# Kernel optimization log

Hardware: AMD Instinct MI355X
Metric: run time of the kernel (lower is better)

The kernel has to match this reference:

```python
import jax, jax.numpy as jnp
import numpy as np

B, S, D_IN = 1, 1024, 2048
H_QK, H_V, DK, DV = 8, 16, 128, 128
KCONV = 4
D_OUT = H_QK * DK          # 1024
D_OUT_VG = H_V * DV        # 2048
FUSED = 2 * D_OUT + D_OUT_VG  # 4096
EPS = 1e-6


def setup_inputs() -> dict:
    key = jax.random.key(0)
    ks = jax.random.split(key, 8)
    return {
        "x": jax.random.normal(ks[0], (B, S, D_IN), jnp.float32),
        "w_qkv": jax.random.normal(ks[1], (FUSED, D_IN), jnp.float32) * 0.02,
        "w_gate": jax.random.normal(ks[2], (D_OUT_VG, D_IN), jnp.float32) * 0.02,
        "w_beta": jax.random.normal(ks[3], (H_V, D_IN), jnp.float32) * 0.02,
        "w_alpha": jax.random.normal(ks[4], (H_V, D_IN), jnp.float32) * 0.02,
        "log_A": jnp.log(jax.random.uniform(ks[5], (H_V,), jnp.float32, 1e-3, 16.0)),
        "dt_bias": jnp.ones((H_V,), jnp.float32),
        "conv_w": jax.random.normal(ks[6], (FUSED, 1, KCONV), jnp.float32) * 0.1,
        "rms_w": jnp.ones((DV,), jnp.float32),
        "w_out": jax.random.normal(ks[7], (D_IN, D_OUT_VG), jnp.float32) * 0.02,
    }


def l2_norm(t):
    return t / jnp.sqrt(jnp.sum(t * t, axis=-1, keepdims=True) + EPS)


def rms_norm(t, w):
    var = jnp.mean(t * t, axis=-1, keepdims=True)
    return t * jax.lax.rsqrt(var + EPS) * w


def gated_delta_rule(q, k, v, beta, alpha):
    # q,k: (b,h,s,dk)  v: (b,h,s,dv)  beta,alpha: (b,h,s)
    q = q * (q.shape[-1] ** -0.5)
    S0 = jnp.zeros(q.shape[:2] + (q.shape[-1], v.shape[-1]), q.dtype)

    def step(Sm, inp):
        q_t, k_t, v_t, b_t, a_t = inp  # (b,h,dk) (b,h,dk) (b,h,dv) (b,h) (b,h)
        Sm = Sm * a_t[..., None, None]                      # decay state
        kv = jnp.einsum('bhk,bhkv->bhv', k_t, Sm)           # k^T S
        u = (v_t - kv) * b_t[..., None]                     # delta-rule target
        Sm = Sm + k_t[..., None] * u[:, :, None, :]         # rank-1 update
        o = jnp.einsum('bhk,bhkv->bhv', q_t, Sm)
        return Sm, o

    xs = (jnp.moveaxis(q, 2, 0), jnp.moveaxis(k, 2, 0), jnp.moveaxis(v, 2, 0),
          jnp.moveaxis(beta, 2, 0), jnp.moveaxis(alpha, 2, 0))
    Sf, outs = jax.lax.scan(step, S0, xs)
    return jnp.moveaxis(outs, 0, 2), Sf  # (b,h,s,dv)


def reference(x, w_qkv, w_gate, w_beta, w_alpha, log_A, dt_bias, conv_w, rms_w, w_out):
    b, seq_len, _ = x.shape
    fused_qkv = x @ w_qkv.T                                  # (b,s,FUSED)
    beta = jax.nn.sigmoid(x @ w_beta.T).transpose(0, 2, 1)   # (b,h_v,s)
    token_projs = x @ w_alpha.T                              # (b,s,h_v)
    alpha = jnp.exp(-jnp.exp(log_A) * jax.nn.softplus(token_projs + dt_bias))
    alpha = alpha.transpose(0, 2, 1)                         # (b,h_v,s)

    # causal depthwise conv1d (padding k-1, truncate to seq_len) + SiLU
    conv_in = fused_qkv.transpose(0, 2, 1)                   # (b,C,s)
    conv_out = jax.lax.conv_general_dilated(
        conv_in, conv_w, window_strides=(1,), padding=[(KCONV - 1, 0)],
        dimension_numbers=('NCH', 'OIH', 'NCH'), feature_group_count=FUSED)
    fused_qkv = jax.nn.silu(conv_out).transpose(0, 2, 1)     # (b,s,C)

    query = fused_qkv[..., :D_OUT].reshape(b, seq_len, H_QK, DK).transpose(0, 2, 1, 3)
    key = fused_qkv[..., D_OUT:2 * D_OUT].reshape(b, seq_len, H_QK, DK).transpose(0, 2, 1, 3)
    value = fused_qkv[..., 2 * D_OUT:].reshape(b, seq_len, H_V, DV).transpose(0, 2, 1, 3)

    query, key = l2_norm(query), l2_norm(key)
    rep = H_V // H_QK
    if rep > 1:
        query = jnp.repeat(query, rep, axis=1)
        key = jnp.repeat(key, rep, axis=1)

    ctx, _ = gated_delta_rule(query, key, value, beta, alpha)  # (b,h_v,s,dv)
    ctx = rms_norm(ctx.astype(jnp.float32), rms_w)
    ctx = ctx.transpose(0, 2, 1, 3).reshape(b, seq_len, D_OUT_VG)

    gate = jax.nn.silu(x @ w_gate.T)
    return (gate * ctx) @ w_out.T
```

## Files before the change

kernel.cpp:

```cpp
#include <hip/hip_runtime.h>

#define AS1 __attribute__((address_space(1)))
#define AS3 __attribute__((address_space(3)))

typedef _Float16 f16x8 __attribute__((ext_vector_type(8)));
typedef _Float16 f16x4 __attribute__((ext_vector_type(4)));
typedef _Float16 f16x2 __attribute__((ext_vector_type(2)));
typedef float f32x4 __attribute__((ext_vector_type(4)));

#define MFMA16(a, b, c) __builtin_amdgcn_mfma_f32_16x16x32_f16((a), (b), (c), 0, 0, 0)

__device__ __forceinline__ float silu_f(float v) { return v / (1.f + expf(-v)); }

__device__ __forceinline__ void gload_lds16(const void* g, void* l) {
    __builtin_amdgcn_global_load_lds((AS1 void*)g, (AS3 void*)l, 16, 0, 0);
}

__global__ __launch_bounds__(256) void cvt_proj(const float* __restrict__ x,
                                                const float* __restrict__ w_qkv,
                                                const float* __restrict__ w_gate,
                                                const float* __restrict__ w_out,
                                                _Float16* __restrict__ dst,
                                                const float* __restrict__ w_beta,
                                                const float* __restrict__ w_alpha,
                                                const float* __restrict__ log_A,
                                                const float* __restrict__ dt_bias,
                                                float* __restrict__ betaB,
                                                float* __restrict__ lalphaB) {
    __shared__ float xs[2048];
    const int bid = blockIdx.x, tid = threadIdx.x;
    if (bid < 18432) {
        long i = ((long)bid * 256 + tid) * 4;
        const float* src; long off;
        if (i < 2097152)       { src = x;      off = 0; }
        else if (i < 10485760) { src = w_qkv;  off = 2097152; }
        else if (i < 14680064) { src = w_gate; off = 10485760; }
        else                   { src = w_out;  off = 14680064; }
        float4 v = *(const float4*)&src[i - off];
        f16x4 h = { (_Float16)v.x, (_Float16)v.y, (_Float16)v.z, (_Float16)v.w };
        *(f16x4*)&dst[i] = h;
        return;
    }
    const int s = bid - 18432;
    *(float4*)&xs[tid * 8]     = *(const float4*)&x[(long)s * 2048 + tid * 8];
    *(float4*)&xs[tid * 8 + 4] = *(const float4*)&x[(long)s * 2048 + tid * 8 + 4];
    __syncthreads();
    const int o = tid >> 3, j = tid & 7;
    const float* w = (o < 16) ? &w_beta[(long)o * 2048] : &w_alpha[(long)(o - 16) * 2048];
    float p = 0.f;
#pragma unroll 4
    for (int i = 0; i < 64; i++) {
        int d = i * 32 + j * 4;
        float4 wv = *(const float4*)&w[d];
        p += xs[d] * wv.x + xs[d + 1] * wv.y + xs[d + 2] * wv.z + xs[d + 3] * wv.w;
    }
    p += __shfl_xor(p, 1); p += __shfl_xor(p, 2); p += __shfl_xor(p, 4);
    if (j == 0) {
        if (o < 16) {
            betaB[s * 16 + o] = 1.f / (1.f + expf(-p));
        } else {
            int h = o - 16;
            float t = p + dt_bias[h];
            float sp = (t > 20.f) ? t : log1pf(expf(t));
            lalphaB[s * 16 + h] = -expf(log_A[h]) * sp;
        }
    }
}

__global__ __launch_bounds__(256) void gemm_bt64h(const _Float16* __restrict__ A,
                                                  const _Float16* __restrict__ B,
                                                  _Float16* __restrict__ C, int N, int K) {
    __shared__ _Float16 S[192 * 32];
    const int tid = threadIdx.x;
    const int rowA0 = blockIdx.y * 64, rowB0 = blockIdx.x * 128;
    const int lane = tid & 63;
    const int wv = tid >> 6;
    const int rw = (wv & 1) * 32, cw = (wv >> 1) * 64;
    const int fr = lane & 15, kof = (lane >> 4) * 8;

    const _Float16* gp[3];
#pragma unroll
    for (int i = 0; i < 3; i++) {
        int u = tid + 256 * i;
        int row = u >> 2, c0 = (u & 3) * 8;
        gp[i] = (row < 64) ? A + (long)(rowA0 + row) * K + c0
                           : B + (long)(rowB0 + row - 64) * K + c0;
    }

    f32x4 zero = {0.f, 0.f, 0.f, 0.f};
    f32x4 acc[2][4];
#pragma unroll
    for (int mi = 0; mi < 2; mi++)
#pragma unroll
        for (int ni = 0; ni < 4; ni++) acc[mi][ni] = zero;

    for (int k0 = 0; k0 < K; k0 += 32) {
        __syncthreads();
#pragma unroll
        for (int i = 0; i < 3; i++)
            gload_lds16(gp[i] + k0, &S[(tid + 256 * i) * 8]);
        __syncthreads();
        f16x8 af[2], bf[4];
#pragma unroll
        for (int mi = 0; mi < 2; mi++) af[mi] = *(const f16x8*)&S[(rw + mi * 16 + fr) * 32 + kof];
#pragma unroll
        for (int ni = 0; ni < 4; ni++) bf[ni] = *(const f16x8*)&S[(64 + cw + ni * 16 + fr) * 32 + kof];
#pragma unroll
        for (int mi = 0; mi < 2; mi++)
#pragma unroll
            for (int ni = 0; ni < 4; ni++)
                acc[mi][ni] = MFMA16(af[mi], bf[ni], acc[mi][ni]);
    }
    const int rbase = (lane >> 4) * 4;
#pragma unroll
    for (int mi = 0; mi < 2; mi++)
#pragma unroll
        for (int ni = 0; ni < 4; ni++) {
            int row = rowA0 + rw + mi * 16 + rbase;
            int col = rowB0 + cw + ni * 16 + fr;
#pragma unroll
            for (int r = 0; r < 4; r++)
                C[(long)(row + r) * N + col] = (_Float16)acc[mi][ni][r];
        }
}

__global__ __launch_bounds__(256) void gemm_bt6464(const _Float16* __restrict__ A,
                                                   const _Float16* __restrict__ B,
                                                   float* __restrict__ C, int N, int K) {
    __shared__ _Float16 S[128 * 32];
    const int tid = threadIdx.x;
    const int rowA0 = blockIdx.y * 64, rowB0 = blockIdx.x * 64;
    const int lane = tid & 63;
    const int wv = tid >> 6;
    const int rw = (wv & 1) * 32, cwol = (wv >> 1) * 32;
    const int fr = lane & 15, kof = (lane >> 4) * 8;

    const _Float16* gp[2];
#pragma unroll
    for (int i = 0; i < 2; i++) {
        int u = tid + 256 * i;
        int row = u >> 2, c0 = (u & 3) * 8;
        gp[i] = (row < 64) ? A + (long)(rowA0 + row) * K + c0
                           : B + (long)(rowB0 + row - 64) * K + c0;
    }

    f32x4 zero = {0.f, 0.f, 0.f, 0.f};
    f32x4 acc[2][2];
#pragma unroll
    for (int mi = 0; mi < 2; mi++)
#pragma unroll
        for (int ni = 0; ni < 2; ni++) acc[mi][ni] = zero;

    for (int k0 = 0; k0 < K; k0 += 32) {
        __syncthreads();
#pragma unroll
        for (int i = 0; i < 2; i++)
            gload_lds16(gp[i] + k0, &S[(tid + 256 * i) * 8]);
        __syncthreads();
        f16x8 af[2], bf[2];
#pragma unroll
        for (int mi = 0; mi < 2; mi++) af[mi] = *(const f16x8*)&S[(rw + mi * 16 + fr) * 32 + kof];
#pragma unroll
        for (int ni = 0; ni < 2; ni++) bf[ni] = *(const f16x8*)&S[(64 + cwol + ni * 16 + fr) * 32 + kof];
#pragma unroll
        for (int mi = 0; mi < 2; mi++)
#pragma unroll
            for (int ni = 0; ni < 2; ni++)
                acc[mi][ni] = MFMA16(af[mi], bf[ni], acc[mi][ni]);
    }
    const int rbase = (lane >> 4) * 4;
#pragma unroll
    for (int mi = 0; mi < 2; mi++)
#pragma unroll
        for (int ni = 0; ni < 2; ni++) {
            int row = rowA0 + rw + mi * 16 + rbase;
            int col = rowB0 + cwol + ni * 16 + fr;
#pragma unroll
            for (int r = 0; r < 4; r++)
                C[(long)(row + r) * N + col] = acc[mi][ni][r];
        }
}

__global__ __launch_bounds__(256) void chunk_front(const _Float16* __restrict__ pre,
                                                   const float* __restrict__ cw,
                                                   const float* __restrict__ betaB,
                                                   const float* __restrict__ lalphaB,
                                                   _Float16* __restrict__ Mw,
                                                   _Float16* __restrict__ QTw,
                                                   _Float16* __restrict__ KTw,
                                                   _Float16* __restrict__ WTw,
                                                   _Float16* __restrict__ Bw,
                                                   _Float16* __restrict__ BTw,
                                                   float* __restrict__ gamC) {
    __shared__ _Float16 Kh[64 * 128];
    __shared__ _Float16 Qh[64 * 128];
    __shared__ _Float16 Vh[64 * 128];
    __shared__ _Float16 Tl[64 * 64];
    __shared__ float lg[64], betL[64], bgamL[64];
    const int hc = blockIdx.x, h = hc >> 4, c = hc & 15, hq = h >> 1, s0 = c * 64;
    const int tid = threadIdx.x;

    if (tid < 64) {
        float la = lalphaB[(s0 + tid) * 16 + h];
#pragma unroll
        for (int d = 1; d < 64; d <<= 1) {
            float tv = __shfl_up(la, d, 64);
            if (tid >= d) la += tv;
        }
        lg[tid] = la;
        float b = betaB[(s0 + tid) * 16 + h];
        betL[tid] = b;
        bgamL[tid] = b * expf(la);
        if (tid == 63) gamC[hc] = expf(la);
    }

    {
        const int tt = tid >> 2, pp = tid & 3, m0 = pp * 32;
        const _Float16* rp[4];
        bool ok0, ok1, ok2;
        {
            int sb = s0 + tt - 3;
            ok0 = (sb >= 0); ok1 = (sb + 1 >= 0); ok2 = (sb + 2 >= 0);
            rp[0] = pre + (long)sb * 6144;
            rp[1] = pre + (long)(sb + 1) * 6144;
            rp[2] = pre + (long)(sb + 2) * 6144;
            rp[3] = pre + (long)(sb + 3) * 6144;
        }
#pragma unroll
        for (int sel = 0; sel < 3; sel++) {
            const int colbase = (sel == 0) ? hq * 128 : (sel == 1) ? 1024 + hq * 128
                                                                   : 2048 + h * 128;
            float vals[32];
            float ss = 0.f;
#pragma unroll
            for (int g = 0; g < 4; g++) {
                const int co = colbase + m0 + g * 8;
                f16x8 r0 = {}, r1 = {}, r2 = {}, r3;
                if (ok0) r0 = *(const f16x8*)&rp[0][co];
                if (ok1) r1 = *(const f16x8*)&rp[1][co];
                if (ok2) r2 = *(const f16x8*)&rp[2][co];
                r3 = *(const f16x8*)&rp[3][co];
#pragma unroll
                for (int j = 0; j < 8; j++) {
                    float4 w = *(const float4*)&cw[(co + j) * 4];
                    float a = (float)r0[j] * w.x + (float)r1[j] * w.y +
                              (float)r2[j] * w.z + (float)r3[j] * w.w;
                    a = silu_f(a);
                    vals[g * 8 + j] = a;
                    ss += a * a;
                }
            }
            float sc = 1.f;
            if (sel < 2) {
                ss += __shfl_xor(ss, 1); ss += __shfl_xor(ss, 2);
                sc = rsqrtf(ss + 1e-6f);
                if (sel == 0) sc *= 0.08838834764831843f;
            }
            _Float16* dst = (sel == 0) ? Qh : (sel == 1) ? Kh : Vh;
#pragma unroll
            for (int g = 0; g < 4; g++) {
                f16x8 hv;
#pragma unroll
                for (int j = 0; j < 8; j++) hv[j] = (_Float16)(vals[g * 8 + j] * sc);
                *(f16x8*)&dst[tt * 128 + m0 + g * 8] = hv;
            }
        }
    }
    __syncthreads();

    for (int e = tid; e < 8192; e += 256) {
        int t = e >> 7;
        QTw[(long)hc * 8192 + e] = (_Float16)(expf(lg[t]) * (float)Qh[e]);
    }
    {
        float lg63 = lg[63];
        for (int e = tid; e < 8192; e += 256) {
            int m = e >> 6, t = e & 63;
            KTw[(long)hc * 8192 + e] = (_Float16)(expf(lg63 - lg[t]) * (float)Kh[t * 128 + m]);
        }
    }

    const int wv = tid >> 6, lane = tid & 63, fr = lane & 15, kof = (lane >> 4) * 8, quad = lane >> 4;
    {
        f32x4 accT[4], accM[4];
        f32x4 zero = {0.f, 0.f, 0.f, 0.f};
#pragma unroll
        for (int ci = 0; ci < 4; ci++) { accT[ci] = zero; accM[ci] = zero; }
        for (int k0 = 0; k0 < 128; k0 += 32) {
            f16x8 ak = *(const f16x8*)&Kh[(wv * 16 + fr) * 128 + k0 + kof];
            f16x8 aq = *(const f16x8*)&Qh[(wv * 16 + fr) * 128 + k0 + kof];
#pragma unroll
            for (int ci = 0; ci < 4; ci++) {
                f16x8 bk = *(const f16x8*)&Kh[(ci * 16 + fr) * 128 + k0 + kof];
                accT[ci] = MFMA16(ak, bk, accT[ci]);
                accM[ci] = MFMA16(aq, bk, accM[ci]);
            }
        }
#pragma unroll
        for (int ci = 0; ci < 4; ci++)
#pragma unroll
            for (int r = 0; r < 4; r++) {
                int t = wv * 16 + quad * 4 + r, i = ci * 16 + fr;
                float e = expf(lg[t] - lg[i]);
                Tl[t * 64 + i] = (_Float16)((i < t) ? betL[t] * e * accT[ci][r] : 0.f);
                Mw[(long)hc * 4096 + t * 64 + i] = (_Float16)((i <= t) ? e * accM[ci][r] : 0.f);
            }
    }
    __syncthreads();

    {
        const int jcol = tid & 127;
        const int halfsel = tid >> 7;
        _Float16* X = halfsel ? Kh : Vh;
        const float* dscale = halfsel ? bgamL : betL;
        float Xa[16];
        for (int a = 0; a < 4; ++a) {
#pragma unroll
            for (int r = 0; r < 16; ++r) {
                int t = a * 16 + r;
                Xa[r] = dscale[t] * (float)X[t * 128 + jcol];
            }
            for (int b = 0; b < a; ++b) {
                float xk[16];
#pragma unroll
                for (int k = 0; k < 16; ++k) xk[k] = (float)X[(b * 16 + k) * 128 + jcol];
#pragma unroll
                for (int k = 0; k < 16; ++k)
#pragma unroll
                    for (int r = 0; r < 16; ++r)
                        Xa[r] -= (float)Tl[(a * 16 + r) * 64 + b * 16 + k] * xk[k];
            }
#pragma unroll
            for (int tp = 0; tp < 16; ++tp) {
                float xt = Xa[tp];
#pragma unroll
                for (int sp = 0; sp < 16; ++sp)
                    if (sp > tp) Xa[sp] -= (float)Tl[(a * 16 + sp) * 64 + a * 16 + tp] * xt;
            }
#pragma unroll
            for (int r = 0; r < 16; ++r) X[(a * 16 + r) * 128 + jcol] = (_Float16)Xa[r];
        }
        if (halfsel == 0) {
            for (int t = 0; t < 64; ++t)
                WTw[((long)hc * 128 + jcol) * 64 + t] = Vh[t * 128 + jcol];
        } else {
            for (int t = 0; t < 64; ++t) {
                _Float16 v = Kh[t * 128 + jcol];
                Bw[(long)hc * 8192 + t * 128 + jcol] = v;
                BTw[((long)hc * 128 + jcol) * 64 + t] = v;
            }
        }
    }
}

__global__ __launch_bounds__(256) void gr_kernel(const _Float16* __restrict__ KTw,
                                                 const _Float16* __restrict__ BTw,
                                                 const _Float16* __restrict__ WTw,
                                                 _Float16* __restrict__ Gw,
                                                 float* __restrict__ Rtw) {
    __shared__ _Float16 KTl[128 * 72], BTl[128 * 72], WTl[128 * 72];
    const long hc = blockIdx.x;
    const int tid = threadIdx.x;
    {
        int r = tid >> 1, c0 = (tid & 1) * 32;
        const _Float16* k_ = &KTw[hc * 8192 + r * 64 + c0];
        const _Float16* b_ = &BTw[hc * 8192 + r * 64 + c0];
        const _Float16* w_ = &WTw[hc * 8192 + r * 64 + c0];
#pragma unroll
        for (int i = 0; i < 4; i++) {
            *(f16x8*)&KTl[r * 72 + c0 + i * 8] = *(const f16x8*)&k_[i * 8];
            *(f16x8*)&BTl[r * 72 + c0 + i * 8] = *(const f16x8*)&b_[i * 8];
            *(f16x8*)&WTl[r * 72 + c0 + i * 8] = *(const f16x8*)&w_[i * 8];
        }
    }
    __syncthreads();
    const int wv = tid >> 6, lane = tid & 63;
    const int fr = lane & 15, kof = (lane >> 4) * 8, quad = lane >> 4;
    f32x4 zero = {0.f, 0.f, 0.f, 0.f};
#pragma unroll
    for (int mi = 0; mi < 2; mi++) {
        int m0 = (wv * 2 + mi) * 16;
        f16x8 a0 = *(const f16x8*)&KTl[(m0 + fr) * 72 + kof];
        f16x8 a1 = *(const f16x8*)&KTl[(m0 + fr) * 72 + 32 + kof];
#pragma unroll
        for (int nj = 0; nj < 8; nj++) {
            f32x4 acc = zero;
            acc = MFMA16(a0, *(const f16x8*)&BTl[(nj * 16 + fr) * 72 + kof], acc);
            acc = MFMA16(a1, *(const f16x8*)&BTl[(nj * 16 + fr) * 72 + 32 + kof], acc);
#pragma unroll
            for (int r = 0; r < 4; r++)
                Gw[hc * 16384 + (long)(m0 + quad * 4 + r) * 128 + nj * 16 + fr] = (_Float16)acc[r];
        }
    }
#pragma unroll
    for (int ji = 0; ji < 2; ji++) {
        int j0 = (wv * 2 + ji) * 16;
        f16x8 a0 = *(const f16x8*)&WTl[(j0 + fr) * 72 + kof];
        f16x8 a1 = *(const f16x8*)&WTl[(j0 + fr) * 72 + 32 + kof];
#pragma unroll
        for (int nm = 0; nm < 8; nm++) {
            f32x4 acc = zero;
            acc = MFMA16(a0, *(const f16x8*)&KTl[(nm * 16 + fr) * 72 + kof], acc);
            acc = MFMA16(a1, *(const f16x8*)&KTl[(nm * 16 + fr) * 72 + 32 + kof], acc);
#pragma unroll
            for (int r = 0; r < 4; r++)
                Rtw[hc * 16384 + (long)(j0 + quad * 4 + r) * 128 + nm * 16 + fr] = acc[r];
        }
    }
}

__global__ __launch_bounds__(256) void serial_scan(const _Float16* __restrict__ Gw,
                                                   const float* __restrict__ Rtw,
                                                   const float* __restrict__ gamC,
                                                   float* __restrict__ Zdump) {
    __shared__ _Float16 Zhi[32 * 136], Zlo[32 * 136];
    __shared__ _Float16 Gl[128 * 136];
    const int tid = threadIdx.x;
    const int h = blockIdx.x >> 2, js = (blockIdx.x & 3) * 32;
    const int wv = tid >> 6, lane = tid & 63;
    const int fr = lane & 15, kof = (lane >> 4) * 8, quad = lane >> 4;
    const int gr_ = tid >> 1, gc_ = (tid & 1) * 64;

    for (int e = tid; e < 32 * 136; e += 256) { Zhi[e] = (_Float16)0.f; Zlo[e] = (_Float16)0.f; }
    float z[2][2][4];
#pragma unroll
    for (int jt = 0; jt < 2; jt++)
#pragma unroll
        for (int u = 0; u < 2; u++)
#pragma unroll
            for (int r = 0; r < 4; r++) z[jt][u][r] = 0.f;

    long hc0 = (long)h * 16;
    f16x8 gpre[8];
#pragma unroll
    for (int i = 0; i < 8; i++)
        gpre[i] = *(const f16x8*)&Gw[hc0 * 16384 + (long)gr_ * 128 + gc_ + i * 8];
    float rpre[2][2][4];
#pragma unroll
    for (int jt = 0; jt < 2; jt++)
#pragma unroll
        for (int u = 0; u < 2; u++)
#pragma unroll
            for (int r = 0; r < 4; r++)
                rpre[jt][u][r] = Rtw[hc0 * 16384 +
                                     (long)(js + jt * 16 + quad * 4 + r) * 128 +
                                     (2 * wv + u) * 16 + fr];
    __syncthreads();

    for (int c = 0; c < 16; ++c) {
        long hc = (long)h * 16 + c;
        float gC = gamC[hc];
#pragma unroll
        for (int i = 0; i < 8; i++)
            *(f16x8*)&Gl[gr_ * 136 + gc_ + i * 8] = gpre[i];
        long hcn = (long)h * 16 + (c < 15 ? c + 1 : 15);
        f16x8 gnext[8];
#pragma unroll
        for (int i = 0; i < 8; i++)
            gnext[i] = *(const f16x8*)&Gw[hcn * 16384 + (long)gr_ * 128 + gc_ + i * 8];
        float rnext[2][2][4];
#pragma unroll
        for (int jt = 0; jt < 2; jt++)
#pragma unroll
            for (int u = 0; u < 2; u++)
#pragma unroll
                for (int r = 0; r < 4; r++)
                    rnext[jt][u][r] = Rtw[hcn * 16384 +
                                          (long)(js + jt * 16 + quad * 4 + r) * 128 +
                                          (2 * wv + u) * 16 + fr];
        __syncthreads();
        f32x4 acc[2][2];
        f32x4 zero = {0.f, 0.f, 0.f, 0.f};
#pragma unroll
        for (int jt = 0; jt < 2; jt++)
#pragma unroll
            for (int u = 0; u < 2; u++) acc[jt][u] = zero;
        for (int k0 = 0; k0 < 128; k0 += 32) {
            f16x8 ahi[2], alo[2], bfr[2];
#pragma unroll
            for (int jt = 0; jt < 2; jt++) {
                ahi[jt] = *(const f16x8*)&Zhi[(jt * 16 + fr) * 136 + k0 + kof];
                alo[jt] = *(const f16x8*)&Zlo[(jt * 16 + fr) * 136 + k0 + kof];
            }
#pragma unroll
            for (int u = 0; u < 2; u++)
                bfr[u] = *(const f16x8*)&Gl[((2 * wv + u) * 16 + fr) * 136 + k0 + kof];
#pragma unroll
            for (int jt = 0; jt < 2; jt++)
#pragma unroll
                for (int u = 0; u < 2; u++) {
                    acc[jt][u] = MFMA16(ahi[jt], bfr[u], acc[jt][u]);
                    acc[jt][u] = MFMA16(alo[jt], bfr[u], acc[jt][u]);
                }
        }
        __syncthreads();
#pragma unroll
        for (int jt = 0; jt < 2; jt++)
#pragma unroll
            for (int u = 0; u < 2; u++)
#pragma unroll
                for (int r = 0; r < 4; r++) {
                    int j = jt * 16 + quad * 4 + r;
                    int m = (2 * wv + u) * 16 + fr;
                    Zdump[hc * 16384 + (long)(js + j) * 128 + m] = z[jt][u][r];
                    float zn = gC * z[jt][u][r] - acc[jt][u][r] + rpre[jt][u][r];
                    z[jt][u][r] = zn;
                    _Float16 hi = (_Float16)zn;
                    Zhi[j * 136 + m] = hi;
                    Zlo[j * 136 + m] = (_Float16)(zn - (float)hi);
                }
#pragma unroll
        for (int i = 0; i < 8; i++) gpre[i] = gnext[i];
#pragma unroll
        for (int jt = 0; jt < 2; jt++)
#pragma unroll
            for (int u = 0; u < 2; u++)
#pragma unroll
                for (int r = 0; r < 4; r++) rpre[jt][u][r] = rnext[jt][u][r];
    }
}

__global__ __launch_bounds__(256) void out_chunk(const float* __restrict__ Zdump,
                                                 const _Float16* __restrict__ Bw,
                                                 const _Float16* __restrict__ WTw,
                                                 const _Float16* __restrict__ QTw,
                                                 const _Float16* __restrict__ Mw,
                                                 float* __restrict__ ctx) {
    __shared__ _Float16 SThi[64 * 136], STlo[64 * 136], Bl[64 * 136];
    __shared__ _Float16 UT[64 * 72];
    const int bid = blockIdx.x;
    const long hc = bid >> 1;
    const int jh = (bid & 1) * 64;
    const int h = (int)(hc >> 4), c = (int)(hc & 15), s0 = c * 64;
    const int tid = threadIdx.x, wv = tid >> 6, lane = tid & 63;
    const int fr = lane & 15, kof = (lane >> 4) * 8, quad = lane >> 4;
    {
        int r = tid >> 2, c0 = (tid & 3) * 32;
        const float* src = &Zdump[hc * 16384 + (long)(jh + r) * 128 + c0];
#pragma unroll
        for (int i = 0; i < 8; i++) {
            float4 v = *(const float4*)&src[i * 4];
            _Float16 h0 = (_Float16)v.x, h1 = (_Float16)v.y, h2 = (_Float16)v.z, h3 = (_Float16)v.w;
            f16x4 hi = {h0, h1, h2, h3};
            f16x4 lo = {(_Float16)(v.x - (float)h0), (_Float16)(v.y - (float)h1),
                        (_Float16)(v.z - (float)h2), (_Float16)(v.w - (float)h3)};
            *(f16x4*)&SThi[r * 136 + c0 + i * 4] = hi;
            *(f16x4*)&STlo[r * 136 + c0 + i * 4] = lo;
        }
        const _Float16* bsrc = &Bw[hc * 8192 + r * 128 + c0];
#pragma unroll
        for (int i = 0; i < 4; i++)
            *(f16x8*)&Bl[r * 136 + c0 + i * 8] = *(const f16x8*)&bsrc[i * 8];
    }
    __syncthreads();
    const int t0 = wv * 16;
    f16x8 ba[4];
#pragma unroll
    for (int k = 0; k < 4; k++)
        ba[k] = *(const f16x8*)&Bl[(t0 + fr) * 136 + k * 32 + kof];
#pragma unroll
    for (int jt = 0; jt < 4; jt++) {
        f32x4 acc = {0.f, 0.f, 0.f, 0.f};
#pragma unroll
        for (int k = 0; k < 4; k++) {
            acc = MFMA16(ba[k], *(const f16x8*)&SThi[(jt * 16 + fr) * 136 + k * 32 + kof], acc);
            acc = MFMA16(ba[k], *(const f16x8*)&STlo[(jt * 16 + fr) * 136 + k * 32 + kof], acc);
        }
#pragma unroll
        for (int r = 0; r < 4; r++) {
            int t = t0 + quad * 4 + r;
            int j = jt * 16 + fr;
            float w = (float)WTw[hc * 8192 + (long)(jh + j) * 64 + t];
            UT[j * 72 + t] = (_Float16)(w - acc[r]);
        }
    }
    __syncthreads();
    f16x8 qa[4], ma[2];
#pragma unroll
    for (int k = 0; k < 4; k++)
        qa[k] = *(const f16x8*)&QTw[hc * 8192 + (long)(t0 + fr) * 128 + k * 32 + kof];
#pragma unroll
    for (int k = 0; k < 2; k++)
        ma[k] = *(const f16x8*)&Mw[hc * 4096 + (long)(t0 + fr) * 64 + k * 32 + kof];
#pragma unroll
    for (int jt = 0; jt < 4; jt++) {
        f32x4 acc = {0.f, 0.f, 0.f, 0.f};
#pragma unroll
        for (int k = 0; k < 4; k++) {
            acc = MFMA16(qa[k], *(const f16x8*)&SThi[(jt * 16 + fr) * 136 + k * 32 + kof], acc);
            acc = MFMA16(qa[k], *(const f16x8*)&STlo[(jt * 16 + fr) * 136 + k * 32 + kof], acc);
        }
#pragma unroll
        for (int k = 0; k < 2; k++)
            acc = MFMA16(ma[k], *(const f16x8*)&UT[(jt * 16 + fr) * 72 + k * 32 + kof], acc);
#pragma unroll
        for (int r = 0; r < 4; r++) {
            int t = t0 + quad * 4 + r;
            int j = jt * 16 + fr;
            ctx[(long)(s0 + t) * 2048 + h * 128 + jh + j] = acc[r];
        }
    }
}

__global__ void epilogue_k(const float* __restrict__ ctx, const _Float16* __restrict__ pre,
                           const float* __restrict__ rms_w, _Float16* __restrict__ y) {
    int gw = (blockIdx.x * blockDim.x + threadIdx.x) >> 6;
    int lane = threadIdx.x & 63;
    int s = gw >> 4, h = gw & 15;
    long base = (long)s * 2048 + h * 128;
    long gbase = (long)s * 6144 + 4096 + h * 128;
    float2 cv = *(const float2*)&ctx[base + lane * 2];
    float ss = cv.x * cv.x + cv.y * cv.y;
#pragma unroll
    for (int m = 1; m < 64; m <<= 1) ss += __shfl_xor(ss, m);
    float sc = rsqrtf(ss * (1.f / 128.f) + 1e-6f);
    int d = lane * 2;
    float2 rw = *(const float2*)&rms_w[d];
    f16x2 gv = *(const f16x2*)&pre[gbase + d];
    float g0 = silu_f((float)gv[0]);
    float g1 = silu_f((float)gv[1]);
    f16x2 hv = { (_Float16)(cv.x * sc * rw.x * g0), (_Float16)(cv.y * sc * rw.y * g1) };
    *(f16x2*)&y[base + d] = hv;
}

extern "C" void kernel_launch(void* const* d_in, const int* in_sizes, int n_in,
                              void* d_out, int out_size, void* d_ws, size_t ws_size,
                              hipStream_t stream) {
    const float* x       = (const float*)d_in[0];
    const float* w_qkv   = (const float*)d_in[1];
    const float* w_gate  = (const float*)d_in[2];
    const float* w_beta  = (const float*)d_in[3];
    const float* w_alpha = (const float*)d_in[4];
    const float* log_A   = (const float*)d_in[5];
    const float* dt_bias = (const float*)d_in[6];
    const float* conv_w  = (const float*)d_in[7];
    const float* rms_w   = (const float*)d_in[8];
    const float* w_out   = (const float*)d_in[9];
    float* outp = (float*)d_out;

    char* ws = (char*)d_ws;
    size_t off = 0;
    _Float16* xb     = (_Float16*)(ws + off); off += (size_t)1024 * 2048 * 2;
    _Float16* wfused = (_Float16*)(ws + off); off += (size_t)6144 * 2048 * 2;
    _Float16* woutb  = (_Float16*)(ws + off); off += (size_t)2048 * 2048 * 2;
    _Float16* yb     = (_Float16*)(ws + off); off += (size_t)1024 * 2048 * 2;
    _Float16* pre    = (_Float16*)(ws + off); off += (size_t)1024 * 6144 * 2;
    float* ctx       = (float*)(ws + off);    off += (size_t)1024 * 16 * 128 * 4;
    float* betaB     = (float*)(ws + off);    off += (size_t)1024 * 16 * 4;
    float* lalphaB   = (float*)(ws + off);    off += (size_t)1024 * 16 * 4;
    _Float16* Mw     = (_Float16*)(ws + off); off += (size_t)256 * 4096 * 2;
    _Float16* QTw    = (_Float16*)(ws + off); off += (size_t)256 * 8192 * 2;
    _Float16* KTw    = (_Float16*)(ws + off); off += (size_t)256 * 8192 * 2;
    _Float16* WTw    = (_Float16*)(ws + off); off += (size_t)256 * 8192 * 2;
    _Float16* Bw     = (_Float16*)(ws + off); off += (size_t)256 * 8192 * 2;
    _Float16* BTw    = (_Float16*)(ws + off); off += (size_t)256 * 8192 * 2;
    float* gamC      = (float*)(ws + off);    off += (size_t)256 * 4;
    _Float16* Gw     = (_Float16*)(ws + off); off += (size_t)256 * 16384 * 2;
    float* Rtw       = (float*)(ws + off);    off += (size_t)256 * 16384 * 4;
    float* Zdump     = (float*)(ws + off);    off += (size_t)256 * 16384 * 4;

    cvt_proj<<<19456, 256, 0, stream>>>(x, w_qkv, w_gate, w_out, xb,
                                        w_beta, w_alpha, log_A, dt_bias, betaB, lalphaB);

    gemm_bt64h<<<dim3(48, 16), 256, 0, stream>>>(xb, wfused, pre, 6144, 2048);

    chunk_front<<<256, 256, 0, stream>>>(pre, conv_w, betaB, lalphaB,
                                         Mw, QTw, KTw, WTw, Bw, BTw, gamC);
    gr_kernel<<<256, 256, 0, stream>>>(KTw, BTw, WTw, Gw, Rtw);
    serial_scan<<<64, 256, 0, stream>>>(Gw, Rtw, gamC, Zdump);
    out_chunk<<<512, 256, 0, stream>>>(Zdump, Bw, WTw, QTw, Mw, ctx);

    epilogue_k<<<4096, 256, 0, stream>>>(ctx, pre, rms_w, yb);
    gemm_bt6464<<<dim3(32, 16), 256, 0, stream>>>(yb, woutb, outp, 2048, 2048);
}
```

Baseline: 316.8 us.

## Restructure chunk_front with 512 threads, padded LDS, and register-resident triangular solve

Doubles the chunk_front block to 512 threads. Warps are split so that four compute the K·K^T (T matrix) MFMAs while four compute Q·K^T (M matrix), and later four run the triangular solve while four write the decayed QT/KT outputs concurrently. LDS rows are padded (136/72) to reduce bank conflicts. The forward substitution keeps all 64 values per column in registers, reading Tl rows vectorised, and its results are written directly with vectorised transposed stores instead of re-reading LDS. Costs include heavier register pressure (64-float array per thread at 512-thread launch bounds) and possible spills.

```diff
diff --git a/kernel.cpp b/kernel.cpp
--- a/kernel.cpp
+++ b/kernel.cpp
@@ -181,7 +181,7 @@
         }
 }
 
-__global__ __launch_bounds__(256) void chunk_front(const _Float16* __restrict__ pre,
+__global__ __launch_bounds__(512) void chunk_front(const _Float16* __restrict__ pre,
                                                    const float* __restrict__ cw,
                                                    const float* __restrict__ betaB,
                                                    const float* __restrict__ lalphaB,
@@ -192,11 +192,11 @@
                                                    _Float16* __restrict__ Bw,
                                                    _Float16* __restrict__ BTw,
                                                    float* __restrict__ gamC) {
-    __shared__ _Float16 Kh[64 * 128];
-    __shared__ _Float16 Qh[64 * 128];
-    __shared__ _Float16 Vh[64 * 128];
-    __shared__ _Float16 Tl[64 * 64];
-    __shared__ float lg[64], betL[64], bgamL[64];
+    __shared__ _Float16 Kh[64 * 136];
+    __shared__ _Float16 Qh[64 * 136];
+    __shared__ _Float16 Vh[64 * 136];
+    __shared__ _Float16 Tl[64 * 72];
+    __shared__ float lg[64], betL[64], bgamL[64], egQ[64], egKr[64];
     const int hc = blockIdx.x, h = hc >> 4, c = hc & 15, hq = h >> 1, s0 = c * 64;
     const int tid = threadIdx.x;
 
@@ -208,14 +208,18 @@
             if (tid >= d) la += tv;
         }
         lg[tid] = la;
+        float la63 = __shfl(la, 63, 64);
         float b = betaB[(s0 + tid) * 16 + h];
+        float eg = expf(la);
         betL[tid] = b;
-        bgamL[tid] = b * expf(la);
-        if (tid == 63) gamC[hc] = expf(la);
+        bgamL[tid] = b * eg;
+        egQ[tid] = eg;
+        egKr[tid] = expf(la63 - la);
+        if (tid == 63) gamC[hc] = eg;
     }
 
     {
-        const int tt = tid >> 2, pp = tid & 3, m0 = pp * 32;
+        const int tt = tid >> 3, pp = tid & 7, m0 = pp * 16;
         const _Float16* rp[4];
         bool ok0, ok1, ok2;
         {
@@ -230,10 +234,10 @@
         for (int sel = 0; sel < 3; sel++) {
             const int colbase = (sel == 0) ? hq * 128 : (sel == 1) ? 1024 + hq * 128
                                                                    : 2048 + h * 128;
-            float vals[32];
+            float vals[16];
             float ss = 0.f;
 #pragma unroll
-            for (int g = 0; g < 4; g++) {
+            for (int g = 0; g < 2; g++) {
                 const int co = colbase + m0 + g * 8;
                 f16x8 r0 = {}, r1 = {}, r2 = {}, r3;
                 if (ok0) r0 = *(const f16x8*)&rp[0][co];
@@ -252,103 +256,146 @@
             }
             float sc = 1.f;
             if (sel < 2) {
-                ss += __shfl_xor(ss, 1); ss += __shfl_xor(ss, 2);
+                ss += __shfl_xor(ss, 1); ss += __shfl_xor(ss, 2); ss += __shfl_xor(ss, 4);
                 sc = rsqrtf(ss + 1e-6f);
                 if (sel == 0) sc *= 0.08838834764831843f;
             }
             _Float16* dst = (sel == 0) ? Qh : (sel == 1) ? Kh : Vh;
 #pragma unroll
-            for (int g = 0; g < 4; g++) {
+            for (int g = 0; g < 2; g++) {
                 f16x8 hv;
 #pragma unroll
                 for (int j = 0; j < 8; j++) hv[j] = (_Float16)(vals[g * 8 + j] * sc);
-                *(f16x8*)&dst[tt * 128 + m0 + g * 8] = hv;
+                *(f16x8*)&dst[tt * 136 + m0 + g * 8] = hv;
             }
         }
     }
     __syncthreads();
 
-    for (int e = tid; e < 8192; e += 256) {
-        int t = e >> 7;
-        QTw[(long)hc * 8192 + e] = (_Float16)(expf(lg[t]) * (float)Qh[e]);
-    }
+    const int wv = tid >> 6, lane = tid & 63;
+    const int fr = lane & 15, kof = (lane >> 4) * 8, quad = lane >> 4;
     {
-        float lg63 = lg[63];
-        for (int e = tid; e < 8192; e += 256) {
-            int m = e >> 6, t = e & 63;
-            KTw[(long)hc * 8192 + e] = (_Float16)(expf(lg63 - lg[t]) * (float)Kh[t * 128 + m]);
-        }
-    }
-
-    const int wv = tid >> 6, lane = tid & 63, fr = lane & 15, kof = (lane >> 4) * 8, quad = lane >> 4;
-    {
-        f32x4 accT[4], accM[4];
         f32x4 zero = {0.f, 0.f, 0.f, 0.f};
-#pragma unroll
-        for (int ci = 0; ci < 4; ci++) { accT[ci] = zero; accM[ci] = zero; }
-        for (int k0 = 0; k0 < 128; k0 += 32) {
-            f16x8 ak = *(const f16x8*)&Kh[(wv * 16 + fr) * 128 + k0 + kof];
-            f16x8 aq = *(const f16x8*)&Qh[(wv * 16 + fr) * 128 + k0 + kof];
-#pragma unroll
-            for (int ci = 0; ci < 4; ci++) {
-                f16x8 bk = *(const f16x8*)&Kh[(ci * 16 + fr) * 128 + k0 + kof];
-                accT[ci] = MFMA16(ak, bk, accT[ci]);
-                accM[ci] = MFMA16(aq, bk, accM[ci]);
-            }
-        }
-#pragma unroll
-        for (int ci = 0; ci < 4; ci++)
-#pragma unroll
-            for (int r = 0; r < 4; r++) {
-                int t = wv * 16 + quad * 4 + r, i = ci * 16 + fr;
-                float e = expf(lg[t] - lg[i]);
-                Tl[t * 64 + i] = (_Float16)((i < t) ? betL[t] * e * accT[ci][r] : 0.f);
-                Mw[(long)hc * 4096 + t * 64 + i] = (_Float16)((i <= t) ? e * accM[ci][r] : 0.f);
-            }
+        if (wv < 4) {
+            f32x4 accT[4];
+#pragma unroll
+            for (int ci = 0; ci < 4; ci++) accT[ci] = zero;
+            for (int k0 = 0; k0 < 128; k0 += 32) {
+                f16x8 ak = *(const f16x8*)&Kh[(wv * 16 + fr) * 136 + k0 + kof];
+#pragma unroll
+                for (int ci = 0; ci < 4; ci++)
+                    accT[ci] = MFMA16(ak, *(const f16x8*)&Kh[(ci * 16 + fr) * 136 + k0 + kof], accT[ci]);
+            }
+#pragma unroll
+            for (int ci = 0; ci < 4; ci++)
+#pragma unroll
+                for (int r = 0; r < 4; r++) {
+                    int t = wv * 16 + quad * 4 + r, i = ci * 16 + fr;
+                    float e = expf(lg[t] - lg[i]);
+                    Tl[t * 72 + i] = (_Float16)((i < t) ? betL[t] * e * accT[ci][r] : 0.f);
+                }
+        } else {
+            const int w = wv - 4;
+            f32x4 accM[4];
+#pragma unroll
+            for (int ci = 0; ci < 4; ci++) accM[ci] = zero;
+            for (int k0 = 0; k0 < 128; k0 += 32) {
+                f16x8 aq = *(const f16x8*)&Qh[(w * 16 + fr) * 136 + k0 + kof];
+#pragma unroll
+                for (int ci = 0; ci < 4; ci++)
+                    accM[ci] = MFMA16(aq, *(const f16x8*)&Kh[(ci * 16 + fr) * 136 + k0 + kof], accM[ci]);
+            }
+#pragma unroll
+            for (int ci = 0; ci < 4; ci++)
+#pragma unroll
+                for (int r = 0; r < 4; r++) {
+                    int t = w * 16 + quad * 4 + r, i = ci * 16 + fr;
+                    float e = expf(lg[t] - lg[i]);
+                    Mw[(long)hc * 4096 + t * 64 + i] = (_Float16)((i <= t) ? e * accM[ci][r] : 0.f);
+                }
+        }
     }
     __syncthreads();
 
-    {
+    if (wv < 4) {
         const int jcol = tid & 127;
-        const int halfsel = tid >> 7;
-        _Float16* X = halfsel ? Kh : Vh;
-        const float* dscale = halfsel ? bgamL : betL;
-        float Xa[16];
-        for (int a = 0; a < 4; ++a) {
-#pragma unroll
-            for (int r = 0; r < 16; ++r) {
-                int t = a * 16 + r;
-                Xa[r] = dscale[t] * (float)X[t * 128 + jcol];
-            }
-            for (int b = 0; b < a; ++b) {
-                float xk[16];
-#pragma unroll
-                for (int k = 0; k < 16; ++k) xk[k] = (float)X[(b * 16 + k) * 128 + jcol];
-#pragma unroll
-                for (int k = 0; k < 16; ++k)
-#pragma unroll
-                    for (int r = 0; r < 16; ++r)
-                        Xa[r] -= (float)Tl[(a * 16 + r) * 64 + b * 16 + k] * xk[k];
-            }
-#pragma unroll
-            for (int tp = 0; tp < 16; ++tp) {
-                float xt = Xa[tp];
-#pragma unroll
-                for (int sp = 0; sp < 16; ++sp)
-                    if (sp > tp) Xa[sp] -= (float)Tl[(a * 16 + sp) * 64 + a * 16 + tp] * xt;
-            }
-#pragma unroll
-            for (int r = 0; r < 16; ++r) X[(a * 16 + r) * 128 + jcol] = (_Float16)Xa[r];
-        }
-        if (halfsel == 0) {
-            for (int t = 0; t < 64; ++t)
-                WTw[((long)hc * 128 + jcol) * 64 + t] = Vh[t * 128 + jcol];
+        const _Float16* Xsrc = (wv < 2) ? Vh : Kh;
+        const float* dscale = (wv < 2) ? betL : bgamL;
+        float Xs[64];
+#pragma unroll
+        for (int t = 0; t < 64; t++) Xs[t] = dscale[t] * (float)Xsrc[t * 136 + jcol];
+#pragma unroll
+        for (int a = 0; a < 4; a++) {
+#pragma unroll
+            for (int b = 0; b < a; b++) {
+#pragma unroll
+                for (int r = 0; r < 16; r++) {
+                    const _Float16* trow = &Tl[(a * 16 + r) * 72 + b * 16];
+                    f16x8 t0 = *(const f16x8*)trow;
+                    f16x8 t1 = *(const f16x8*)(trow + 8);
+                    float acc = 0.f;
+#pragma unroll
+                    for (int k = 0; k < 8; k++) acc += (float)t0[k] * Xs[b * 16 + k];
+#pragma unroll
+                    for (int k = 0; k < 8; k++) acc += (float)t1[k] * Xs[b * 16 + 8 + k];
+                    Xs[a * 16 + r] -= acc;
+                }
+            }
+#pragma unroll
+            for (int sp = 1; sp < 16; sp++) {
+                const _Float16* trow = &Tl[(a * 16 + sp) * 72 + a * 16];
+                f16x8 t0 = *(const f16x8*)trow;
+                f16x8 t1 = *(const f16x8*)(trow + 8);
+                float acc = 0.f;
+#pragma unroll
+                for (int tp = 0; tp < 16; tp++) {
+                    if (tp < sp) acc += (float)(tp < 8 ? t0[tp] : t1[tp - 8]) * Xs[a * 16 + tp];
+                }
+                Xs[a * 16 + sp] -= acc;
+            }
+        }
+        if (wv < 2) {
+#pragma unroll
+            for (int v = 0; v < 8; v++) {
+                f16x8 hv;
+#pragma unroll
+                for (int j = 0; j < 8; j++) hv[j] = (_Float16)Xs[v * 8 + j];
+                *(f16x8*)&WTw[((long)hc * 128 + jcol) * 64 + v * 8] = hv;
+            }
         } else {
-            for (int t = 0; t < 64; ++t) {
-                _Float16 v = Kh[t * 128 + jcol];
-                Bw[(long)hc * 8192 + t * 128 + jcol] = v;
-                BTw[((long)hc * 128 + jcol) * 64 + t] = v;
-            }
+#pragma unroll
+            for (int t = 0; t < 64; t++) Bw[(long)hc * 8192 + t * 128 + jcol] = (_Float16)Xs[t];
+#pragma unroll
+            for (int v = 0; v < 8; v++) {
+                f16x8 hv;
+#pragma unroll
+                for (int j = 0; j < 8; j++) hv[j] = (_Float16)Xs[v * 8 + j];
+                *(f16x8*)&BTw[((long)hc * 128 + jcol) * 64 + v * 8] = hv;
+            }
+        }
+    } else {
+        const int w = wv - 4;
+#pragma unroll
+        for (int cp = 0; cp < 4; cp++) {
+            int t = w * 16 + fr;
+            int cc = cp * 32 + kof;
+            f16x8 q = *(const f16x8*)&Qh[t * 136 + cc];
+            float s = egQ[t];
+            f16x8 o;
+#pragma unroll
+            for (int j = 0; j < 8; j++) o[j] = (_Float16)(s * (float)q[j]);
+            *(f16x8*)&QTw[(long)hc * 8192 + t * 128 + cc] = o;
+        }
+        const int m = w * 32 + (lane & 31);
+        const int tb = (lane >> 5) * 8;
+#pragma unroll
+        for (int tp = 0; tp < 4; tp++) {
+            int t0 = tb + tp * 16;
+            f16x8 o;
+#pragma unroll
+            for (int j = 0; j < 8; j++)
+                o[j] = (_Float16)(egKr[t0 + j] * (float)Kh[(t0 + j) * 136 + m]);
+            *(f16x8*)&KTw[(long)hc * 8192 + m * 64 + t0] = o;
         }
     }
 }
@@ -664,7 +711,7 @@
 
     gemm_bt64h<<<dim3(48, 16), 256, 0, stream>>>(xb, wfused, pre, 6144, 2048);
 
-    chunk_front<<<256, 256, 0, stream>>>(pre, conv_w, betaB, lalphaB,
+    chunk_front<<<256, 512, 0, stream>>>(pre, conv_w, betaB, lalphaB,
                                          Mw, QTw, KTw, WTw, Bw, BTw, gamC);
     gr_kernel<<<256, 256, 0, stream>>>(KTw, BTw, WTw, Gw, Rtw);
     serial_scan<<<64, 256, 0, stream>>>(Gw, Rtw, gamC, Zdump);
```

Result: faster. 298.0 us (-5.9%).
